# Performance work log

Measured on AMD Instinct MI355X. Metric: run time of the kernel, lower is better.

## Reference

```python
import jax, jax.numpy as jnp
import numpy as np

N_NODES = 50000


def setup_inputs() -> dict:
    key = jax.random.key(0)
    k1, k2, k3, k4, k5 = jax.random.split(key, 5)
    x = jax.random.normal(k1, (N_NODES, 128), dtype=jnp.float32)
    edge_index = jax.random.randint(k2, (1600000, 2), 0, N_NODES, dtype=jnp.int64)
    # learned params for the concrete combine: out = agg @ W_neigh + self @ W_self + b
    W_neigh = jax.random.normal(k3, (128, 128), dtype=jnp.float32) * (1.0 / np.sqrt(128))
    W_self = jax.random.normal(k4, (128, 128), dtype=jnp.float32) * (1.0 / np.sqrt(128))
    b = jax.random.normal(k5, (128,), dtype=jnp.float32) * 0.01
    return {"x": x, "edge_index": edge_index, "W_neigh": W_neigh, "W_self": W_self, "b": b}


def reference(x, edge_index, W_neigh, W_self, b):
    n = x.shape[0]
    src = edge_index[:, 0]
    dst = edge_index[:, 1]
    # undirected: each edge (i,j) sends x[j] -> i and x[i] -> j
    agg_sum = jax.ops.segment_sum(x[dst], src, num_segments=n)
    agg_sum = agg_sum + jax.ops.segment_sum(x[src], dst, num_segments=n)
    ones = jnp.ones((edge_index.shape[0],), dtype=x.dtype)
    deg = jax.ops.segment_sum(ones, src, num_segments=n)
    deg = deg + jax.ops.segment_sum(ones, dst, num_segments=n)
    agg_mean = agg_sum / jnp.maximum(deg, 1.0)[:, None]  # mean aggregate
    # combine(agg, self)
    return agg_mean @ W_neigh + x @ W_self + b
```

## Files before the change

### kernel.cpp

```cpp
#include <hip/hip_runtime.h>
#include <hip/hip_fp16.h>


constexpr int DIM    = 128;
constexpr int NBMAX  = 512;
constexpr int EPB    = 2048;
constexpr int CAP    = 9216;
constexpr int COLT   = 32;
constexpr int NTILES = DIM / COLT;

typedef _Float16 half8 __attribute__((ext_vector_type(8)));
typedef __attribute__((ext_vector_type(4))) float f32x4;

__device__ __forceinline__ unsigned hadd2u(unsigned a, unsigned b) {
    __half2 ha = *reinterpret_cast<__half2*>(&a);
    __half2 hb = *reinterpret_cast<__half2*>(&b);
    __half2 r  = __hadd2(ha, hb);
    return *reinterpret_cast<unsigned*>(&r);
}
__device__ __forceinline__ unsigned hmul2u(unsigned a, __half2 s) {
    __half2 ha = *reinterpret_cast<__half2*>(&a);
    __half2 r  = __hmul2(ha, s);
    return *reinterpret_cast<unsigned*>(&r);
}
__device__ __forceinline__ unsigned packf16(float x, float y) {
    __half2 h = __floats2half2_rn(x, y);
    return *reinterpret_cast<unsigned*>(&h);
}

__global__ __launch_bounds__(256) void k_packw_init(
    const float* __restrict__ Wn, const float* __restrict__ Ws,
    unsigned short* __restrict__ Bp, int* __restrict__ bucket_cur, int nb)
{
    int i = blockIdx.x * 256 + threadIdx.x;
    if (i < nb) bucket_cur[i] = i * CAP;
    if (i >= 8 * 128 * 4 * 8) return;
    int j    = i & 7;
    int quad = (i >> 3) & 3;
    int n    = (i >> 5) & 127;
    int kb   = i >> 12;
    int k = kb * 32 + quad * 8 + j;
    float v = (k < 128) ? Wn[k * 128 + n] : Ws[(k - 128) * 128 + n];
    __half h = __float2half_rn(v);
    Bp[i] = *reinterpret_cast<unsigned short*>(&h);
}

__global__ __launch_bounds__(256) void k_bin(
    const int* __restrict__ edge, int* __restrict__ bucket_cur,
    unsigned* __restrict__ entries, int n_edges, int nb)
{
    __shared__ int lh[4][NBMAX];
    __shared__ int Lb[NBMAX];
    __shared__ int gb[NBMAX];
    __shared__ int sc[512];
    __shared__ unsigned sorted[2 * EPB];
    __shared__ int      gaddr[2 * EPB];

    int t = threadIdx.x;
    int w = t >> 6;
    for (int i = t; i < 4 * NBMAX; i += 256) ((int*)lh)[i] = 0;
    __syncthreads();

    int e0 = blockIdx.x * EPB;
    int2 ev[8];
    #pragma unroll
    for (int k = 0; k < 8; k++) {
        int idx = e0 + k * 256 + t;
        if (idx < n_edges) {
            ev[k] = ((const int2*)edge)[idx];
            atomicAdd(&lh[w][ev[k].x >> 7], 1);
            atomicAdd(&lh[w][ev[k].y >> 7], 1);
        } else {
            ev[k].x = -1;
        }
    }
    __syncthreads();

    for (int i = t; i < 512; i += 256)
        sc[i] = (i < nb) ? (lh[0][i] + lh[1][i] + lh[2][i] + lh[3][i]) : 0;
    __syncthreads();
    for (int d = 1; d < 512; d <<= 1) {
        int v0 = 0, v1 = 0;
        int i0 = t, i1 = t + 256;
        if (i0 >= d) v0 = sc[i0 - d];
        if (i1 >= d) v1 = sc[i1 - d];
        __syncthreads();
        if (i0 >= d) sc[i0] += v0;
        if (i1 >= d) sc[i1] += v1;
        __syncthreads();
    }
    for (int i = t; i < nb; i += 256) {
        int c0 = lh[0][i], c1 = lh[1][i], c2 = lh[2][i], c3 = lh[3][i];
        int tot = c0 + c1 + c2 + c3;
        int L = sc[i] - tot;
        Lb[i] = L;
        gb[i] = tot ? atomicAdd(&bucket_cur[i], tot) : 0;
        lh[0][i] = L;
        lh[1][i] = L + c0;
        lh[2][i] = L + c0 + c1;
        lh[3][i] = L + c0 + c1 + c2;
    }
    __syncthreads();

    #pragma unroll
    for (int k = 0; k < 8; k++) {
        int a = ev[k].x;
        if (a < 0) continue;
        int b = ev[k].y;
        int ba = a >> 7, bb = b >> 7;
        int sa = atomicAdd(&lh[w][ba], 1);
        sorted[sa] = ((unsigned)(a & 127) << 16) | (unsigned)b;
        gaddr[sa]  = gb[ba] + sa - Lb[ba];
        int sb = atomicAdd(&lh[w][bb], 1);
        sorted[sb] = ((unsigned)(b & 127) << 16) | (unsigned)a;
        gaddr[sb]  = gb[bb] + sb - Lb[bb];
    }
    __syncthreads();

    int cntb = sc[511];
    for (int p = t; p < cntb; p += 256)
        entries[gaddr[p]] = sorted[p];
}

__global__ __launch_bounds__(512) void k_csort(
    const unsigned* __restrict__ entries, const int* __restrict__ bucket_cur,
    unsigned* __restrict__ offsets, int* __restrict__ degs,
    unsigned short* __restrict__ nbr, int n_nodes)
{
    int b    = blockIdx.x;
    int base = b * CAP;
    int cnt  = bucket_cur[b] - base;
    __shared__ int lh[8][128];
    __shared__ int scn[128];
    int t = threadIdx.x;
    int w = t >> 6;
    for (int i = t; i < 8 * 128; i += 512) ((int*)lh)[i] = 0;
    __syncthreads();
    for (int i = t; i < cnt; i += 512)
        atomicAdd(&lh[w][entries[base + i] >> 16], 1);
    __syncthreads();
    int tot = 0;
    if (t < 128) {
        #pragma unroll
        for (int ww = 0; ww < 8; ww++) tot += lh[ww][t];
        scn[t] = tot;
    }
    __syncthreads();
    for (int d = 1; d < 128; d <<= 1) {
        int u = (t >= d && t < 128) ? scn[t - d] : 0;
        __syncthreads();
        if (t >= d && t < 128) scn[t] += u;
        __syncthreads();
    }
    if (t < 128) {
        int excl = scn[t] - tot;
        int node = (b << 7) + t;
        if (node < n_nodes) {
            offsets[node] = (unsigned)(base + excl);
            degs[node]    = tot;
        }
        int run = excl;
        #pragma unroll
        for (int ww = 0; ww < 8; ww++) { int c = lh[ww][t]; lh[ww][t] = run; run += c; }
    }
    __syncthreads();
    for (int i = t; i < cnt; i += 512) {
        unsigned e = entries[base + i];
        int slot = atomicAdd(&lh[w][e >> 16], 1);
        nbr[base + slot] = (unsigned short)(e & 0xFFFFu);
    }
}

__global__ __launch_bounds__(256) void k_tof16t(
    const float* __restrict__ x, unsigned* __restrict__ xt,
    unsigned* __restrict__ abf, int n_nodes)
{
    int i = blockIdx.x * 256 + threadIdx.x;
    int per = n_nodes * 16;
    if (i >= per * NTILES) return;
    int t   = i / per;
    int rem = i - t * per;
    int n   = rem >> 4;
    int u   = rem & 15;
    float2 f = ((const float2*)(x + (size_t)n * DIM + t * COLT))[u];
    unsigned pk = packf16(f.x, f.y);
    xt[i] = pk;
    abf[(size_t)n * 128 + 64 + t * 16 + u] = pk;
}

__global__ __launch_bounds__(256) void k_gather(
    const unsigned* __restrict__ xt,
    const unsigned* __restrict__ offsets,
    const int* __restrict__ degs,
    const unsigned short* __restrict__ nbr,
    unsigned* __restrict__ abf, int n_nodes)
{
    int node = blockIdx.x * 4 + (threadIdx.x >> 6);
    if (node >= n_nodes) return;
    int tile = blockIdx.y;
    const uint4* xt_tile = (const uint4*)(xt + (size_t)tile * n_nodes * 16);
    int lane = threadIdx.x & 63;
    int grp  = lane >> 2;
    int u    = lane & 3;
    int base = (int)offsets[node];
    int deg  = degs[node];
    int end  = base + deg;

    unsigned s0 = 0u, s1 = 0u, s2 = 0u, s3 = 0u;

    int i = base + grp;
    for (; i + 16 < end; i += 32) {
        int v0 = nbr[i];
        int v1 = nbr[i + 16];
        uint4 w0 = xt_tile[v0 * 4 + u];
        uint4 w1 = xt_tile[v1 * 4 + u];
        s0 = hadd2u(s0, w0.x); s1 = hadd2u(s1, w0.y);
        s2 = hadd2u(s2, w0.z); s3 = hadd2u(s3, w0.w);
        s0 = hadd2u(s0, w1.x); s1 = hadd2u(s1, w1.y);
        s2 = hadd2u(s2, w1.z); s3 = hadd2u(s3, w1.w);
    }
    if (i < end) {
        int v0 = nbr[i];
        uint4 w0 = xt_tile[v0 * 4 + u];
        s0 = hadd2u(s0, w0.x); s1 = hadd2u(s1, w0.y);
        s2 = hadd2u(s2, w0.z); s3 = hadd2u(s3, w0.w);
    }

    #pragma unroll
    for (int off = 4; off < 64; off <<= 1) {
        s0 = hadd2u(s0, (unsigned)__shfl_xor((int)s0, off));
        s1 = hadd2u(s1, (unsigned)__shfl_xor((int)s1, off));
        s2 = hadd2u(s2, (unsigned)__shfl_xor((int)s2, off));
        s3 = hadd2u(s3, (unsigned)__shfl_xor((int)s3, off));
    }

    if (grp == 0) {
        float inv = 1.0f / fmaxf((float)deg, 1.0f);
        __half2 iv = __float2half2_rn(inv);
        uint4 o;
        o.x = hmul2u(s0, iv);
        o.y = hmul2u(s1, iv);
        o.z = hmul2u(s2, iv);
        o.w = hmul2u(s3, iv);
        ((uint4*)(abf + (size_t)node * 128 + tile * 16))[u] = o;
    }
}

__global__ __launch_bounds__(256) void k_mfma_gemm(
    const unsigned short* __restrict__ abf,
    const unsigned short* __restrict__ Bp,
    const float* __restrict__ bias,
    float* __restrict__ out, int n_nodes)
{
    int wave = threadIdx.x >> 6;
    int lane = threadIdx.x & 63;
    int quad = lane >> 4;
    int l16  = lane & 15;
    int row0 = blockIdx.x * 64 + wave * 16;

    int arow = min(row0 + l16, n_nodes - 1);
    const unsigned short* arp = abf + (size_t)arow * 256 + quad * 8;
    half8 afrag[8];
    #pragma unroll
    for (int kb = 0; kb < 8; kb++)
        afrag[kb] = *((const half8*)(arp + kb * 32));

    f32x4 acc[8];
    #pragma unroll
    for (int f = 0; f < 8; f++) acc[f] = (f32x4){0.f, 0.f, 0.f, 0.f};

    #pragma unroll
    for (int kb = 0; kb < 8; kb++) {
        #pragma unroll
        for (int f = 0; f < 8; f++) {
            int n = f * 16 + l16;
            half8 bfrag = *((const half8*)(Bp + (((size_t)kb * 128 + n) * 4 + quad) * 8));
            acc[f] = __builtin_amdgcn_mfma_f32_16x16x32_f16(afrag[kb], bfrag, acc[f], 0, 0, 0);
        }
    }

    #pragma unroll
    for (int f = 0; f < 8; f++) {
        float bv = bias[f * 16 + l16];
        #pragma unroll
        for (int r = 0; r < 4; r++) {
            int row = row0 + quad * 4 + r;
            if (row < n_nodes)
                out[(size_t)row * DIM + f * 16 + l16] = acc[f][r] + bv;
        }
    }
}

extern "C" void kernel_launch(void* const* d_in, const int* in_sizes, int n_in,
                              void* d_out, int out_size, void* d_ws, size_t ws_size,
                              hipStream_t stream) {
    const float* x    = (const float*)d_in[0];
    const int*   edge = (const int*)  d_in[1];
    const float* Wn   = (const float*)d_in[2];
    const float* Ws   = (const float*)d_in[3];
    const float* b    = (const float*)d_in[4];
    float* out = (float*)d_out;

    const int n_nodes = in_sizes[0] / DIM;
    const int n_edges = in_sizes[1] / 2;
    const int nb = (n_nodes + 127) >> 7;

    unsigned* entries      = (unsigned*)d_ws;
    unsigned short* nbr    = (unsigned short*)(entries + (size_t)nb * CAP);
    unsigned* offsets      = (unsigned*)(nbr + (size_t)nb * CAP);
    int* degs              = (int*)(offsets + n_nodes);
    int* bucket_cur        = degs + n_nodes;
    unsigned short* Bp     = (unsigned short*)((((size_t)(bucket_cur + nb)) + 63) & ~(size_t)63);
    unsigned* xt           = entries;
    unsigned* abf          = (unsigned*)d_out;

    k_packw_init<<<128, 256, 0, stream>>>(Wn, Ws, Bp, bucket_cur, nb);

    const int bb = (n_edges + EPB - 1) / EPB;
    k_bin<<<bb, 256, 0, stream>>>(edge, bucket_cur, entries, n_edges, nb);
    k_csort<<<nb, 512, 0, stream>>>(entries, bucket_cur, offsets, degs, nbr, n_nodes);

    const int nconv = n_nodes * 16 * NTILES;
    k_tof16t<<<(nconv + 255) / 256, 256, 0, stream>>>(x, xt, abf, n_nodes);

    dim3 ggrid((n_nodes + 3) / 4, NTILES);
    k_gather<<<ggrid, 256, 0, stream>>>(xt, offsets, degs, nbr, abf, n_nodes);

    const int mb = (n_nodes + 63) / 64;
    k_mfma_gemm<<<mb, 256, 0, stream>>>((const unsigned short*)abf, Bp, b,
                                        out, n_nodes);
}
```

Before: 254.1 us.

## Gather full fp16 rows directly from abf instead of column-tiled copy

The separate column-tiled fp16 copy of x and the 4-way tile grid split for the gather are removed. Each wave now gathers full 256-byte neighbor rows straight from the self half of the abf buffer, with 4 neighbor groups of 16 lanes, 4-way unrolled independent accumulators, and a shorter shuffle reduction. This drops one conversion write stream and the index re-reads across tiles. The cost is a larger per-wave working set with less L2 locality per tile, and the gather reads abf while also writing into it (the agg half, so no overlap).

```diff
diff --git a/kernel.cpp b/kernel.cpp
--- a/kernel.cpp
+++ b/kernel.cpp
@@ -6,8 +6,6 @@
 constexpr int NBMAX  = 512;
 constexpr int EPB    = 2048;
 constexpr int CAP    = 9216;
-constexpr int COLT   = 32;
-constexpr int NTILES = DIM / COLT;
 
 typedef _Float16 half8 __attribute__((ext_vector_type(8)));
 typedef __attribute__((ext_vector_type(4))) float f32x4;
@@ -172,24 +170,17 @@
 }
 
 __global__ __launch_bounds__(256) void k_tof16t(
-    const float* __restrict__ x, unsigned* __restrict__ xt,
-    unsigned* __restrict__ abf, int n_nodes)
+    const float* __restrict__ x, unsigned* __restrict__ abf, int n_nodes)
 {
     int i = blockIdx.x * 256 + threadIdx.x;
-    int per = n_nodes * 16;
-    if (i >= per * NTILES) return;
-    int t   = i / per;
-    int rem = i - t * per;
-    int n   = rem >> 4;
-    int u   = rem & 15;
-    float2 f = ((const float2*)(x + (size_t)n * DIM + t * COLT))[u];
-    unsigned pk = packf16(f.x, f.y);
-    xt[i] = pk;
-    abf[(size_t)n * 128 + 64 + t * 16 + u] = pk;
+    if (i >= n_nodes * 64) return;
+    int n = i >> 6;
+    int u = i & 63;
+    float2 f = ((const float2*)(x + (size_t)n * DIM))[u];
+    abf[(size_t)n * 128 + 64 + u] = packf16(f.x, f.y);
 }
 
 __global__ __launch_bounds__(256) void k_gather(
-    const unsigned* __restrict__ xt,
     const unsigned* __restrict__ offsets,
     const int* __restrict__ degs,
     const unsigned short* __restrict__ nbr,
@@ -197,37 +188,51 @@
 {
     int node = blockIdx.x * 4 + (threadIdx.x >> 6);
     if (node >= n_nodes) return;
-    int tile = blockIdx.y;
-    const uint4* xt_tile = (const uint4*)(xt + (size_t)tile * n_nodes * 16);
     int lane = threadIdx.x & 63;
-    int grp  = lane >> 2;
-    int u    = lane & 3;
+    int grp  = lane >> 4;
+    int u    = lane & 15;
+    const uint4* xr = (const uint4*)abf;
     int base = (int)offsets[node];
     int deg  = degs[node];
     int end  = base + deg;
 
-    unsigned s0 = 0u, s1 = 0u, s2 = 0u, s3 = 0u;
+    unsigned p0[4], p1[4], p2[4], p3[4];
+    #pragma unroll
+    for (int d = 0; d < 4; d++) { p0[d] = 0u; p1[d] = 0u; p2[d] = 0u; p3[d] = 0u; }
 
     int i = base + grp;
-    for (; i + 16 < end; i += 32) {
+    for (; i + 12 < end; i += 16) {
         int v0 = nbr[i];
-        int v1 = nbr[i + 16];
-        uint4 w0 = xt_tile[v0 * 4 + u];
-        uint4 w1 = xt_tile[v1 * 4 + u];
-        s0 = hadd2u(s0, w0.x); s1 = hadd2u(s1, w0.y);
-        s2 = hadd2u(s2, w0.z); s3 = hadd2u(s3, w0.w);
-        s0 = hadd2u(s0, w1.x); s1 = hadd2u(s1, w1.y);
-        s2 = hadd2u(s2, w1.z); s3 = hadd2u(s3, w1.w);
-    }
-    if (i < end) {
+        int v1 = nbr[i + 4];
+        int v2 = nbr[i + 8];
+        int v3 = nbr[i + 12];
+        uint4 w0 = xr[v0 * 32 + 16 + u];
+        uint4 w1 = xr[v1 * 32 + 16 + u];
+        uint4 w2 = xr[v2 * 32 + 16 + u];
+        uint4 w3 = xr[v3 * 32 + 16 + u];
+        p0[0] = hadd2u(p0[0], w0.x); p1[0] = hadd2u(p1[0], w0.y);
+        p2[0] = hadd2u(p2[0], w0.z); p3[0] = hadd2u(p3[0], w0.w);
+        p0[1] = hadd2u(p0[1], w1.x); p1[1] = hadd2u(p1[1], w1.y);
+        p2[1] = hadd2u(p2[1], w1.z); p3[1] = hadd2u(p3[1], w1.w);
+        p0[2] = hadd2u(p0[2], w2.x); p1[2] = hadd2u(p1[2], w2.y);
+        p2[2] = hadd2u(p2[2], w2.z); p3[2] = hadd2u(p3[2], w2.w);
+        p0[3] = hadd2u(p0[3], w3.x); p1[3] = hadd2u(p1[3], w3.y);
+        p2[3] = hadd2u(p2[3], w3.z); p3[3] = hadd2u(p3[3], w3.w);
+    }
+    for (; i < end; i += 4) {
         int v0 = nbr[i];
-        uint4 w0 = xt_tile[v0 * 4 + u];
-        s0 = hadd2u(s0, w0.x); s1 = hadd2u(s1, w0.y);
-        s2 = hadd2u(s2, w0.z); s3 = hadd2u(s3, w0.w);
-    }
-
-    #pragma unroll
-    for (int off = 4; off < 64; off <<= 1) {
+        uint4 w0 = xr[v0 * 32 + 16 + u];
+        p0[0] = hadd2u(p0[0], w0.x); p1[0] = hadd2u(p1[0], w0.y);
+        p2[0] = hadd2u(p2[0], w0.z); p3[0] = hadd2u(p3[0], w0.w);
+    }
+
+    unsigned s0 = hadd2u(hadd2u(p0[0], p0[1]), hadd2u(p0[2], p0[3]));
+    unsigned s1 = hadd2u(hadd2u(p1[0], p1[1]), hadd2u(p1[2], p1[3]));
+    unsigned s2 = hadd2u(hadd2u(p2[0], p2[1]), hadd2u(p2[2], p2[3]));
+    unsigned s3 = hadd2u(hadd2u(p3[0], p3[1]), hadd2u(p3[2], p3[3]));
+
+    #pragma unroll
+    for (int off = 16; off < 64; off <<= 1) {
         s0 = hadd2u(s0, (unsigned)__shfl_xor((int)s0, off));
         s1 = hadd2u(s1, (unsigned)__shfl_xor((int)s1, off));
         s2 = hadd2u(s2, (unsigned)__shfl_xor((int)s2, off));
@@ -242,7 +247,7 @@
         o.y = hmul2u(s1, iv);
         o.z = hmul2u(s2, iv);
         o.w = hmul2u(s3, iv);
-        ((uint4*)(abf + (size_t)node * 128 + tile * 16))[u] = o;
+        ((uint4*)(abf + (size_t)node * 128))[u] = o;
     }
 }
 
@@ -311,7 +316,6 @@
     int* degs              = (int*)(offsets + n_nodes);
     int* bucket_cur        = degs + n_nodes;
     unsigned short* Bp     = (unsigned short*)((((size_t)(bucket_cur + nb)) + 63) & ~(size_t)63);
-    unsigned* xt           = entries;
     unsigned* abf          = (unsigned*)d_out;
 
     k_packw_init<<<128, 256, 0, stream>>>(Wn, Ws, Bp, bucket_cur, nb);
@@ -320,11 +324,10 @@
     k_bin<<<bb, 256, 0, stream>>>(edge, bucket_cur, entries, n_edges, nb);
     k_csort<<<nb, 512, 0, stream>>>(entries, bucket_cur, offsets, degs, nbr, n_nodes);
 
-    const int nconv = n_nodes * 16 * NTILES;
-    k_tof16t<<<(nconv + 255) / 256, 256, 0, stream>>>(x, xt, abf, n_nodes);
-
-    dim3 ggrid((n_nodes + 3) / 4, NTILES);
-    k_gather<<<ggrid, 256, 0, stream>>>(xt, offsets, degs, nbr, abf, n_nodes);
+    const int nconv = n_nodes * 64;
+    k_tof16t<<<(nconv + 255) / 256, 256, 0, stream>>>(x, abf, n_nodes);
+
+    k_gather<<<(n_nodes + 3) / 4, 256, 0, stream>>>(offsets, degs, nbr, abf, n_nodes);
 
     const int mb = (n_nodes + 63) / 64;
     k_mfma_gemm<<<mb, 256, 0, stream>>>((const unsigned short*)abf, Bp, b,
```

Measured after the change: 252.4 us. No clear change (-0.7%).

## Assign one node per 4-lane group in gather instead of one wave per node

Applied to the files above, without the earlier changes.

The gather kernel now maps 16 nodes per wave, with each group of 4 lanes handling one node's full neighbor list serially. Previously a whole 64-lane wave handled one node and combined partial sums with cross-lane shuffles. The change removes the shuffle reduction and the idle lanes left by the average degree of about 64 split across 16 groups. It keeps four independent accumulators to overlap loads. The trade-off is load imbalance within a wave, since lanes wait on the highest-degree node, and sequential per-node neighbor index reads that are less coalesced.

```diff
diff --git a/kernel.cpp b/kernel.cpp
--- a/kernel.cpp
+++ b/kernel.cpp
@@ -26,6 +26,14 @@
 __device__ __forceinline__ unsigned packf16(float x, float y) {
     __half2 h = __floats2half2_rn(x, y);
     return *reinterpret_cast<unsigned*>(&h);
+}
+__device__ __forceinline__ uint4 hadd2q(uint4 a, uint4 b) {
+    uint4 r;
+    r.x = hadd2u(a.x, b.x);
+    r.y = hadd2u(a.y, b.y);
+    r.z = hadd2u(a.z, b.z);
+    r.w = hadd2u(a.w, b.w);
+    return r;
 }
 
 __global__ __launch_bounds__(256) void k_packw_init(
@@ -195,53 +203,51 @@
     const unsigned short* __restrict__ nbr,
     unsigned* __restrict__ abf, int n_nodes)
 {
-    int node = blockIdx.x * 4 + (threadIdx.x >> 6);
-    if (node >= n_nodes) return;
-    int tile = blockIdx.y;
-    const uint4* xt_tile = (const uint4*)(xt + (size_t)tile * n_nodes * 16);
+    int wave = threadIdx.x >> 6;
     int lane = threadIdx.x & 63;
     int grp  = lane >> 2;
     int u    = lane & 3;
-    int base = (int)offsets[node];
-    int deg  = degs[node];
-    int end  = base + deg;
-
-    unsigned s0 = 0u, s1 = 0u, s2 = 0u, s3 = 0u;
-
-    int i = base + grp;
-    for (; i + 16 < end; i += 32) {
+    int node = blockIdx.x * 64 + wave * 16 + grp;
+    int tile = blockIdx.y;
+    const uint4* xt_tile = (const uint4*)(xt + (size_t)tile * n_nodes * 16);
+    bool valid = node < n_nodes;
+    int base = 0, deg = 0;
+    if (valid) { base = (int)offsets[node]; deg = degs[node]; }
+    int end = base + deg;
+
+    uint4 s0 = {0u, 0u, 0u, 0u};
+    uint4 s1 = s0, s2 = s0, s3 = s0;
+
+    int i = base;
+    for (; i + 3 < end; i += 4) {
         int v0 = nbr[i];
-        int v1 = nbr[i + 16];
+        int v1 = nbr[i + 1];
+        int v2 = nbr[i + 2];
+        int v3 = nbr[i + 3];
         uint4 w0 = xt_tile[v0 * 4 + u];
         uint4 w1 = xt_tile[v1 * 4 + u];
-        s0 = hadd2u(s0, w0.x); s1 = hadd2u(s1, w0.y);
-        s2 = hadd2u(s2, w0.z); s3 = hadd2u(s3, w0.w);
-        s0 = hadd2u(s0, w1.x); s1 = hadd2u(s1, w1.y);
-        s2 = hadd2u(s2, w1.z); s3 = hadd2u(s3, w1.w);
-    }
-    if (i < end) {
-        int v0 = nbr[i];
-        uint4 w0 = xt_tile[v0 * 4 + u];
-        s0 = hadd2u(s0, w0.x); s1 = hadd2u(s1, w0.y);
-        s2 = hadd2u(s2, w0.z); s3 = hadd2u(s3, w0.w);
-    }
-
-    #pragma unroll
-    for (int off = 4; off < 64; off <<= 1) {
-        s0 = hadd2u(s0, (unsigned)__shfl_xor((int)s0, off));
-        s1 = hadd2u(s1, (unsigned)__shfl_xor((int)s1, off));
-        s2 = hadd2u(s2, (unsigned)__shfl_xor((int)s2, off));
-        s3 = hadd2u(s3, (unsigned)__shfl_xor((int)s3, off));
-    }
-
-    if (grp == 0) {
+        uint4 w2 = xt_tile[v2 * 4 + u];
+        uint4 w3 = xt_tile[v3 * 4 + u];
+        s0 = hadd2q(s0, w0);
+        s1 = hadd2q(s1, w1);
+        s2 = hadd2q(s2, w2);
+        s3 = hadd2q(s3, w3);
+    }
+    for (; i < end; i++) {
+        int v = nbr[i];
+        s0 = hadd2q(s0, xt_tile[v * 4 + u]);
+    }
+
+    uint4 m = hadd2q(hadd2q(s0, s1), hadd2q(s2, s3));
+
+    if (valid) {
         float inv = 1.0f / fmaxf((float)deg, 1.0f);
         __half2 iv = __float2half2_rn(inv);
         uint4 o;
-        o.x = hmul2u(s0, iv);
-        o.y = hmul2u(s1, iv);
-        o.z = hmul2u(s2, iv);
-        o.w = hmul2u(s3, iv);
+        o.x = hmul2u(m.x, iv);
+        o.y = hmul2u(m.y, iv);
+        o.z = hmul2u(m.z, iv);
+        o.w = hmul2u(m.w, iv);
         ((uint4*)(abf + (size_t)node * 128 + tile * 16))[u] = o;
     }
 }
@@ -323,7 +329,7 @@
     const int nconv = n_nodes * 16 * NTILES;
     k_tof16t<<<(nconv + 255) / 256, 256, 0, stream>>>(x, xt, abf, n_nodes);
 
-    dim3 ggrid((n_nodes + 3) / 4, NTILES);
+    dim3 ggrid((n_nodes + 63) / 64, NTILES);
     k_gather<<<ggrid, 256, 0, stream>>>(xt, offsets, degs, nbr, abf, n_nodes);
 
     const int mb = (n_nodes + 63) / 64;
```

New measurement: 309.7 us. 21.9% more time.
